# Kernel optimization log

Measured on AMD Instinct MI355X. Metric: run time of the kernel, lower is better.

## Reference

```python
import jax, jax.numpy as jnp
import numpy as np

N_USERS = 100000
N_MOVIES = 50000
EMB_DIM = 64
N_EDGES = 5000000


def setup_inputs() -> dict:
    key = jax.random.key(0)
    k1, k2, k3 = jax.random.split(key, 3)
    N = N_USERS + N_MOVIES
    edge_index = jax.random.randint(k1, (2, N_EDGES), 0, N, dtype=jnp.int64)
    user_emb = 0.1 * jax.random.normal(k2, (N_USERS, EMB_DIM), dtype=jnp.float32)
    movie_emb = 0.1 * jax.random.normal(k3, (N_MOVIES, EMB_DIM), dtype=jnp.float32)
    return {"edge_index": edge_index, "n_layers": 3,
            "user_emb": user_emb, "movie_emb": movie_emb}


def reference(edge_index, n_layers, user_emb, movie_emb):
    n_users = user_emb.shape[0]
    N = n_users + movie_emb.shape[0]
    x = jnp.concatenate([user_emb, movie_emb], axis=0)  # [N, D]

    row, col = edge_index[0], edge_index[1]  # source -> target
    # gcn_norm without self-loops (LGConv default): deg from target (col)
    deg = jnp.zeros((N,), x.dtype).at[col].add(1.0)
    dis = jnp.where(deg > 0, jax.lax.rsqrt(jnp.maximum(deg, 1.0)), 0.0)
    norm = dis[row] * dis[col]  # [E]

    acc = x
    total = x
    for _ in range(n_layers):
        msg = acc[row] * norm[:, None]            # [E, D] gather + scale
        acc = jax.ops.segment_sum(msg, col, num_segments=N)  # scatter-add
        total = total + acc
    final = total / (n_layers + 1)                # mean over layers 0..K
    return final[:n_users], final[n_users:]
```

## Files before the change

### kernel.cpp

```cpp
#include <hip/hip_runtime.h>

typedef _Float16 half_t;
typedef _Float16 half2_t __attribute__((ext_vector_type(2)));
union pk_u { unsigned int u; half2_t h; };

#define EMB 64
#define NLAYERS 3
#define BSH2 9
#define BW2 512
#define NB2MAX 512
#define CAP 20480
#define P1_BATCH 4096
#define P1_EPT 16

__device__ inline void scan_512(int* __restrict__ hist, int* __restrict__ lstart,
                                int* __restrict__ pair) {
    int t = threadIdx.x;
    int a0 = hist[2 * t], a1 = hist[2 * t + 1];
    pair[t] = a0 + a1;
    __syncthreads();
    for (int off = 1; off < 256; off <<= 1) {
        int u = (t >= off) ? pair[t - off] : 0;
        __syncthreads();
        pair[t] += u;
        __syncthreads();
    }
    lstart[2 * t]     = pair[t] - a0 - a1;
    lstart[2 * t + 1] = pair[t] - a1;
    __syncthreads();
}

__global__ __launch_bounds__(256) void part_kernel(
        const int* __restrict__ row, const int* __restrict__ col,
        int* __restrict__ gcount, int* __restrict__ tmp, int E, int nb2) {
    __shared__ int hist[NB2MAX];
    __shared__ int lstart[NB2MAX];
    __shared__ int gbase[NB2MAX];
    __shared__ int pair[256];
    __shared__ int srec[P1_BATCH];
    __shared__ unsigned short sbuck[P1_BATCH];

    int base = blockIdx.x * P1_BATCH;
    int nE = min(P1_BATCH, E - base);

    for (int i = threadIdx.x; i < NB2MAX; i += 256) hist[i] = 0;
    __syncthreads();

    int myc[P1_EPT];
    #pragma unroll
    for (int k = 0; k < P1_EPT; ++k) {
        int idx = base + (k << 8) + threadIdx.x;
        int c = (idx < E) ? col[idx] : -1;
        myc[k] = c;
        if (c >= 0) atomicAdd(&hist[c >> BSH2], 1);
    }
    __syncthreads();

    scan_512(hist, lstart, pair);

    for (int b = threadIdx.x; b < nb2; b += 256) {
        int c = hist[b];
        int off = 0;
        if (c > 0) off = atomicAdd(&gcount[b], c);
        gbase[b] = b * CAP + off - lstart[b];
    }
    __syncthreads();
    for (int b = threadIdx.x; b < NB2MAX; b += 256) hist[b] = lstart[b];
    __syncthreads();

    #pragma unroll
    for (int k = 0; k < P1_EPT; ++k) {
        int idx = base + (k << 8) + threadIdx.x;
        if (idx < E) {
            int c = myc[k];
            int b = c >> BSH2;
            int r = row[idx];
            int pos = atomicAdd(&hist[b], 1);
            srec[pos] = (r << BSH2) | (c & (BW2 - 1));
            sbuck[pos] = (unsigned short)b;
        }
    }
    __syncthreads();

    for (int i = threadIdx.x; i < nE; i += 256)
        tmp[gbase[sbuck[i]] + i] = srec[i];
}

__global__ __launch_bounds__(256) void bin_kernel(
        const int* __restrict__ tmp, const int* __restrict__ gcount,
        int* __restrict__ eg, int2* __restrict__ sd, float* __restrict__ dis,
        const float4* __restrict__ uev, const float4* __restrict__ mev,
        float4* __restrict__ outv, uint2* __restrict__ s0v,
        int n_users, int N) {
    __shared__ int hist[BW2];
    __shared__ int lstart[BW2];
    __shared__ int pair[256];
    __shared__ float sdis[BW2];
    int b = blockIdx.x;
    int cnt = gcount[b];
    int rbase = b * CAP;
    int c0 = b << BSH2;
    int nc = min(BW2, N - c0);

    for (int i = threadIdx.x; i < BW2; i += 256) hist[i] = 0;
    __syncthreads();
    for (int i = threadIdx.x; i < cnt; i += 256)
        atomicAdd(&hist[tmp[rbase + i] & (BW2 - 1)], 1);
    __syncthreads();

    scan_512(hist, lstart, pair);

    for (int c = threadIdx.x; c < nc; c += 256) {
        int d = hist[c];
        float dn = (d > 0) ? rsqrtf((float)d) : 0.0f;
        sd[c0 + c] = make_int2(rbase + lstart[c], d);
        dis[c0 + c] = dn;
        sdis[c] = dn;
    }
    __syncthreads();
    for (int i = threadIdx.x; i < BW2; i += 256) hist[i] = lstart[i];
    __syncthreads();

    for (int i = threadIdx.x; i < cnt; i += 256) {
        int v = tmp[rbase + i];
        int pos = atomicAdd(&hist[v & (BW2 - 1)], 1);
        eg[rbase + pos] = v >> BSH2;
    }

    for (int i = threadIdx.x; i < nc * 16; i += 256) {
        int loc = i >> 4;
        int node = c0 + loc;
        int q = i & 15;
        const float4* src = (node < n_users) ? (uev + (long long)node * 16)
                                             : (mev + (long long)(node - n_users) * 16);
        float4 v = src[q];
        outv[(long long)node * 16 + q] = v;
        float dn = sdis[loc];
        pk_u w0, w1;
        w0.h[0] = (half_t)(v.x * dn); w0.h[1] = (half_t)(v.y * dn);
        w1.h[0] = (half_t)(v.z * dn); w1.h[1] = (half_t)(v.w * dn);
        s0v[(long long)node * 16 + q] = make_uint2(w0.u, w1.u);
    }
}

template <bool LAST>
__global__ void gather_kernel(const int* __restrict__ eg, const int2* __restrict__ sd,
                              const float* __restrict__ dis,
                              const uint2* __restrict__ tab, uint2* __restrict__ sB,
                              float4* __restrict__ outv, float scale, int N) {
    int wave = blockIdx.x * (blockDim.x >> 6) + (threadIdx.x >> 6);
    if (wave >= N) return;
    int l = threadIdx.x & 63;
    int p = l & 15;
    int h = l >> 4;

    int2 se = sd[wave];
    int j = se.x;
    int e = se.x + se.y;
    pk_u a01, a23;
    a01.u = 0; a23.u = 0;

    for (; j + 15 < e; j += 16) {
        int r0 = eg[j + h];
        int r1 = eg[j + 4 + h];
        int r2 = eg[j + 8 + h];
        int r3 = eg[j + 12 + h];
        uint2 v0 = tab[(long long)r0 * 16 + p];
        uint2 v1 = tab[(long long)r1 * 16 + p];
        uint2 v2 = tab[(long long)r2 * 16 + p];
        uint2 v3 = tab[(long long)r3 * 16 + p];
        pk_u t;
        t.u = v0.x; a01.h += t.h;  t.u = v0.y; a23.h += t.h;
        t.u = v1.x; a01.h += t.h;  t.u = v1.y; a23.h += t.h;
        t.u = v2.x; a01.h += t.h;  t.u = v2.y; a23.h += t.h;
        t.u = v3.x; a01.h += t.h;  t.u = v3.y; a23.h += t.h;
    }
    for (; j < e; j += 4) {
        if (h < e - j) {
            int r0 = eg[j + h];
            uint2 v0 = tab[(long long)r0 * 16 + p];
            pk_u t;
            t.u = v0.x; a01.h += t.h;  t.u = v0.y; a23.h += t.h;
        }
    }

    pk_u t;
    t.u = (unsigned int)__shfl_xor((int)a01.u, 16); a01.h += t.h;
    t.u = (unsigned int)__shfl_xor((int)a01.u, 32); a01.h += t.h;
    t.u = (unsigned int)__shfl_xor((int)a23.u, 16); a23.h += t.h;
    t.u = (unsigned int)__shfl_xor((int)a23.u, 32); a23.h += t.h;

    if (h == 0) {
        float dc = dis[wave];
        float g0 = dc * (float)a01.h[0];
        float g1 = dc * (float)a01.h[1];
        float g2 = dc * (float)a23.h[0];
        float g3 = dc * (float)a23.h[1];
        long long o = (long long)wave * 16 + p;
        float4 v = outv[o];
        v.x = (v.x + g0) * scale;
        v.y = (v.y + g1) * scale;
        v.z = (v.z + g2) * scale;
        v.w = (v.w + g3) * scale;
        outv[o] = v;
        if (!LAST) {
            pk_u w0, w1;
            w0.h[0] = (half_t)(dc * g0); w0.h[1] = (half_t)(dc * g1);
            w1.h[0] = (half_t)(dc * g2); w1.h[1] = (half_t)(dc * g3);
            sB[o] = make_uint2(w0.u, w1.u);
        }
    }
}

extern "C" void kernel_launch(void* const* d_in, const int* in_sizes, int n_in,
                              void* d_out, int out_size, void* d_ws, size_t ws_size,
                              hipStream_t stream) {
    const int*   edge = (const int*)d_in[0];
    const float* ue   = (const float*)d_in[2];
    const float* me   = (const float*)d_in[3];
    float*       out  = (float*)d_out;

    const int E        = in_sizes[0] / 2;
    const int n_users  = in_sizes[2] / EMB;
    const int n_movies = in_sizes[3] / EMB;
    const int N        = n_users + n_movies;
    const int* row = edge;
    const int* col = edge + E;
    const int nb2 = (N + BW2 - 1) >> BSH2;

    char* ws = (char*)d_ws;
    auto align_up = [](size_t v) { return (v + 255) & ~(size_t)255; };
    int*    gcount = (int*)ws;    ws += align_up((size_t)NB2MAX * sizeof(int));
    int2*   sd     = (int2*)ws;   ws += align_up((size_t)N * sizeof(int2));
    float*  dis    = (float*)ws;  ws += align_up((size_t)N * sizeof(float));
    int*    tmp    = (int*)ws;    ws += align_up((size_t)nb2 * CAP * sizeof(int));
    int*    eg     = (int*)ws;    ws += align_up((size_t)nb2 * CAP * sizeof(int));
    half_t* sA     = (half_t*)ws; ws += align_up((size_t)N * EMB * sizeof(half_t));
    half_t* sB     = (half_t*)ws; ws += align_up((size_t)N * EMB * sizeof(half_t));

    hipMemsetAsync(gcount, 0, (size_t)NB2MAX * sizeof(int), stream);
    part_kernel<<<(E + P1_BATCH - 1) / P1_BATCH, 256, 0, stream>>>(
        row, col, gcount, tmp, E, nb2);
    bin_kernel<<<nb2, 256, 0, stream>>>(
        tmp, gcount, eg, sd, dis,
        (const float4*)ue, (const float4*)me, (float4*)out, (uint2*)sA,
        n_users, N);

    const int waves_per_block = 4;
    const int gblocks = (N + waves_per_block - 1) / waves_per_block;
    gather_kernel<false><<<gblocks, 256, 0, stream>>>(
        eg, sd, dis, (const uint2*)sA, (uint2*)sB, (float4*)out, 1.0f, N);
    gather_kernel<false><<<gblocks, 256, 0, stream>>>(
        eg, sd, dis, (const uint2*)sB, (uint2*)sA, (float4*)out, 1.0f, N);
    gather_kernel<true><<<gblocks, 256, 0, stream>>>(
        eg, sd, dis, (const uint2*)sA, (uint2*)sB, (float4*)out,
        1.0f / (NLAYERS + 1), N);
}
```

Baseline: 533.8 us.

## Widen partition/bin blocks and unroll gather to 8 predicated loads per lane

Raises part_kernel to 512 threads and bin_kernel to 1024 threads, adapting the 512-entry scan so only the first 256 threads take part. The bin kernel now stores pre-shifted row indices (row<<4), so the gather kernel can form 32-bit byte offsets without 64-bit multiplies. The gather loop is restructured to issue 8 clamped index loads and 8 table loads per lane per iteration, with predication replacing the separate 16-edge main loop and remainder tail. This aims to expose more memory-level parallelism in the latency-bound gather and cut address arithmetic. In exchange, short adjacency lists do wasted clamped loads, and the 32-bit offsets limit how large the table can be.

```diff
diff --git a/kernel.cpp b/kernel.cpp
--- a/kernel.cpp
+++ b/kernel.cpp
@@ -11,26 +11,31 @@
 #define NB2MAX 512
 #define CAP 20480
 #define P1_BATCH 4096
-#define P1_EPT 16
-
-__device__ inline void scan_512(int* __restrict__ hist, int* __restrict__ lstart,
-                                int* __restrict__ pair) {
+#define P1_TH 512
+#define P1_EPT 8
+#define BINTH 1024
+
+__device__ inline void scan_512w(int* __restrict__ hist, int* __restrict__ lstart,
+                                 int* __restrict__ pair) {
     int t = threadIdx.x;
-    int a0 = hist[2 * t], a1 = hist[2 * t + 1];
-    pair[t] = a0 + a1;
+    int a0 = 0, a1 = 0;
+    if (t < 256) { a0 = hist[2 * t]; a1 = hist[2 * t + 1]; pair[t] = a0 + a1; }
     __syncthreads();
     for (int off = 1; off < 256; off <<= 1) {
-        int u = (t >= off) ? pair[t - off] : 0;
+        int u = 0;
+        if (t < 256 && t >= off) u = pair[t - off];
         __syncthreads();
-        pair[t] += u;
+        if (t < 256) pair[t] += u;
         __syncthreads();
     }
-    lstart[2 * t]     = pair[t] - a0 - a1;
-    lstart[2 * t + 1] = pair[t] - a1;
-    __syncthreads();
-}
-
-__global__ __launch_bounds__(256) void part_kernel(
+    if (t < 256) {
+        lstart[2 * t]     = pair[t] - a0 - a1;
+        lstart[2 * t + 1] = pair[t] - a1;
+    }
+    __syncthreads();
+}
+
+__global__ __launch_bounds__(512) void part_kernel(
         const int* __restrict__ row, const int* __restrict__ col,
         int* __restrict__ gcount, int* __restrict__ tmp, int E, int nb2) {
     __shared__ int hist[NB2MAX];
@@ -43,34 +48,34 @@
     int base = blockIdx.x * P1_BATCH;
     int nE = min(P1_BATCH, E - base);
 
-    for (int i = threadIdx.x; i < NB2MAX; i += 256) hist[i] = 0;
+    for (int i = threadIdx.x; i < NB2MAX; i += P1_TH) hist[i] = 0;
     __syncthreads();
 
     int myc[P1_EPT];
     #pragma unroll
     for (int k = 0; k < P1_EPT; ++k) {
-        int idx = base + (k << 8) + threadIdx.x;
+        int idx = base + (k << 9) + threadIdx.x;
         int c = (idx < E) ? col[idx] : -1;
         myc[k] = c;
         if (c >= 0) atomicAdd(&hist[c >> BSH2], 1);
     }
     __syncthreads();
 
-    scan_512(hist, lstart, pair);
-
-    for (int b = threadIdx.x; b < nb2; b += 256) {
+    scan_512w(hist, lstart, pair);
+
+    for (int b = threadIdx.x; b < nb2; b += P1_TH) {
         int c = hist[b];
         int off = 0;
         if (c > 0) off = atomicAdd(&gcount[b], c);
         gbase[b] = b * CAP + off - lstart[b];
     }
     __syncthreads();
-    for (int b = threadIdx.x; b < NB2MAX; b += 256) hist[b] = lstart[b];
+    for (int b = threadIdx.x; b < NB2MAX; b += P1_TH) hist[b] = lstart[b];
     __syncthreads();
 
     #pragma unroll
     for (int k = 0; k < P1_EPT; ++k) {
-        int idx = base + (k << 8) + threadIdx.x;
+        int idx = base + (k << 9) + threadIdx.x;
         if (idx < E) {
             int c = myc[k];
             int b = c >> BSH2;
@@ -82,11 +87,11 @@
     }
     __syncthreads();
 
-    for (int i = threadIdx.x; i < nE; i += 256)
+    for (int i = threadIdx.x; i < nE; i += P1_TH)
         tmp[gbase[sbuck[i]] + i] = srec[i];
 }
 
-__global__ __launch_bounds__(256) void bin_kernel(
+__global__ __launch_bounds__(1024) void bin_kernel(
         const int* __restrict__ tmp, const int* __restrict__ gcount,
         int* __restrict__ eg, int2* __restrict__ sd, float* __restrict__ dis,
         const float4* __restrict__ uev, const float4* __restrict__ mev,
@@ -102,15 +107,15 @@
     int c0 = b << BSH2;
     int nc = min(BW2, N - c0);
 
-    for (int i = threadIdx.x; i < BW2; i += 256) hist[i] = 0;
-    __syncthreads();
-    for (int i = threadIdx.x; i < cnt; i += 256)
+    for (int i = threadIdx.x; i < BW2; i += BINTH) hist[i] = 0;
+    __syncthreads();
+    for (int i = threadIdx.x; i < cnt; i += BINTH)
         atomicAdd(&hist[tmp[rbase + i] & (BW2 - 1)], 1);
     __syncthreads();
 
-    scan_512(hist, lstart, pair);
-
-    for (int c = threadIdx.x; c < nc; c += 256) {
+    scan_512w(hist, lstart, pair);
+
+    for (int c = threadIdx.x; c < nc; c += BINTH) {
         int d = hist[c];
         float dn = (d > 0) ? rsqrtf((float)d) : 0.0f;
         sd[c0 + c] = make_int2(rbase + lstart[c], d);
@@ -118,16 +123,16 @@
         sdis[c] = dn;
     }
     __syncthreads();
-    for (int i = threadIdx.x; i < BW2; i += 256) hist[i] = lstart[i];
-    __syncthreads();
-
-    for (int i = threadIdx.x; i < cnt; i += 256) {
+    for (int i = threadIdx.x; i < BW2; i += BINTH) hist[i] = lstart[i];
+    __syncthreads();
+
+    for (int i = threadIdx.x; i < cnt; i += BINTH) {
         int v = tmp[rbase + i];
         int pos = atomicAdd(&hist[v & (BW2 - 1)], 1);
-        eg[rbase + pos] = v >> BSH2;
-    }
-
-    for (int i = threadIdx.x; i < nc * 16; i += 256) {
+        eg[rbase + pos] = (v >> BSH2) << 4;
+    }
+
+    for (int i = threadIdx.x; i < nc * 16; i += BINTH) {
         int loc = i >> 4;
         int node = c0 + loc;
         int q = i & 15;
@@ -144,15 +149,18 @@
 }
 
 template <bool LAST>
-__global__ void gather_kernel(const int* __restrict__ eg, const int2* __restrict__ sd,
-                              const float* __restrict__ dis,
-                              const uint2* __restrict__ tab, uint2* __restrict__ sB,
-                              float4* __restrict__ outv, float scale, int N) {
+__global__ __launch_bounds__(256) void gather_kernel(
+        const int* __restrict__ eg, const int2* __restrict__ sd,
+        const float* __restrict__ dis,
+        const uint2* __restrict__ tab, uint2* __restrict__ sB,
+        float4* __restrict__ outv, float scale, int N) {
     int wave = blockIdx.x * (blockDim.x >> 6) + (threadIdx.x >> 6);
     if (wave >= N) return;
     int l = threadIdx.x & 63;
     int p = l & 15;
     int h = l >> 4;
+    unsigned pb = (unsigned)p << 3;
+    const char* tb = (const char*)tab;
 
     int2 se = sd[wave];
     int j = se.x;
@@ -160,27 +168,22 @@
     pk_u a01, a23;
     a01.u = 0; a23.u = 0;
 
-    for (; j + 15 < e; j += 16) {
-        int r0 = eg[j + h];
-        int r1 = eg[j + 4 + h];
-        int r2 = eg[j + 8 + h];
-        int r3 = eg[j + 12 + h];
-        uint2 v0 = tab[(long long)r0 * 16 + p];
-        uint2 v1 = tab[(long long)r1 * 16 + p];
-        uint2 v2 = tab[(long long)r2 * 16 + p];
-        uint2 v3 = tab[(long long)r3 * 16 + p];
-        pk_u t;
-        t.u = v0.x; a01.h += t.h;  t.u = v0.y; a23.h += t.h;
-        t.u = v1.x; a01.h += t.h;  t.u = v1.y; a23.h += t.h;
-        t.u = v2.x; a01.h += t.h;  t.u = v2.y; a23.h += t.h;
-        t.u = v3.x; a01.h += t.h;  t.u = v3.y; a23.h += t.h;
-    }
-    for (; j < e; j += 4) {
-        if (h < e - j) {
-            int r0 = eg[j + h];
-            uint2 v0 = tab[(long long)r0 * 16 + p];
+    for (; j < e; j += 32) {
+        int last = e - 1;
+        int r[8];
+        bool ok[8];
+        #pragma unroll
+        for (int k = 0; k < 8; ++k) {
+            int idx = j + (k << 2) + h;
+            ok[k] = idx < e;
+            r[k] = eg[min(idx, last)];
+        }
+        #pragma unroll
+        for (int k = 0; k < 8; ++k) {
+            uint2 v = *(const uint2*)(tb + ((unsigned)(r[k] << 3) + pb));
             pk_u t;
-            t.u = v0.x; a01.h += t.h;  t.u = v0.y; a23.h += t.h;
+            t.u = ok[k] ? v.x : 0u; a01.h += t.h;
+            t.u = ok[k] ? v.y : 0u; a23.h += t.h;
         }
     }
 
@@ -239,9 +242,9 @@
     half_t* sB     = (half_t*)ws; ws += align_up((size_t)N * EMB * sizeof(half_t));
 
     hipMemsetAsync(gcount, 0, (size_t)NB2MAX * sizeof(int), stream);
-    part_kernel<<<(E + P1_BATCH - 1) / P1_BATCH, 256, 0, stream>>>(
+    part_kernel<<<(E + P1_BATCH - 1) / P1_BATCH, P1_TH, 0, stream>>>(
         row, col, gcount, tmp, E, nb2);
-    bin_kernel<<<nb2, 256, 0, stream>>>(
+    bin_kernel<<<nb2, BINTH, 0, stream>>>(
         tmp, gcount, eg, sd, dis,
         (const float4*)ue, (const float4*)me, (float4*)out, (uint2*)sA,
         n_users, N);
```

New measurement: 497.9 us. 6.7% less time.
